# Kernel tuning notes

Hardware: AMD Instinct MI355X
Metric: run time of the kernel (lower is better)

Reference implementation:

```python
import jax, jax.numpy as jnp
import numpy as np

N_NODES = 100000


def gcn_conv(x, edge_index, weight, num_nodes):
    """PyG GCNConv (bias=False): transform -> add self-loops -> sym-normalized scatter-add."""
    h = x @ weight  # [N, out]
    src, dst = edge_index[0], edge_index[1]
    loop = jnp.arange(num_nodes, dtype=src.dtype)
    src = jnp.concatenate([src, loop])
    dst = jnp.concatenate([dst, loop])
    ones = jnp.ones(src.shape[0], dtype=h.dtype)
    deg = jax.ops.segment_sum(ones, dst, num_segments=num_nodes)  # in-degree incl. self-loop
    dis = jnp.where(deg > 0, jax.lax.rsqrt(deg), 0.0)             # deg^-1/2, inf -> 0
    norm = dis[src] * dis[dst]                                    # [E+N]
    msg = norm[:, None] * h[src]                                  # gather + scale
    return jax.ops.segment_sum(msg, dst, num_segments=num_nodes)  # scatter-add


def setup_inputs() -> dict:
    key = jax.random.key(0)
    k1, k2, k3, k4 = jax.random.split(key, 4)
    x = jax.random.normal(k1, (N_NODES, 512), dtype=jnp.float32)
    edge_index = jax.random.randint(k2, (2, 3200000), 0, N_NODES, dtype=jnp.int64)
    weight1 = jax.random.normal(k3, (512, 16), dtype=jnp.float32) * 0.05
    weight2 = jax.random.normal(k4, (16, 16), dtype=jnp.float32) * 0.25
    return {"x": x, "edge_index": edge_index, "weight1": weight1, "weight2": weight2}


def reference(x, edge_index, weight1, weight2):
    n = x.shape[0]
    h = gcn_conv(x, edge_index, weight1, n)
    out = gcn_conv(h, edge_index, weight2, n)
    return out
```

## Files before the change

kernel.cpp:

```cpp
#include <hip/hip_runtime.h>
#include <hip/hip_bf16.h>


#define N_NODES 100000
#define F_IN 512
#define F_OUT 16

__global__ void k_deg_init(float* __restrict__ deg, int n) {
    int i = blockIdx.x * blockDim.x + threadIdx.x;
    if (i < n) deg[i] = 1.0f;
}

__global__ void k_deg_count(const int* __restrict__ dst, float* __restrict__ deg, int E) {
    int e = blockIdx.x * blockDim.x + threadIdx.x;
    if (e < E) unsafeAtomicAdd(&deg[dst[e]], 1.0f);
}

__global__ void k_rsqrt(float* __restrict__ deg, int n) {
    int i = blockIdx.x * blockDim.x + threadIdx.x;
    if (i < n) deg[i] = rsqrtf(deg[i]);
}

__global__ __launch_bounds__(256) void k_gemm1(const float* __restrict__ x,
                                               const float* __restrict__ W,
                                               float* __restrict__ h, int nrows) {
    __shared__ float Ws[F_IN * F_OUT];
    const float4* W4 = (const float4*)W;
    float4* Ws4 = (float4*)Ws;
    for (int i = threadIdx.x; i < (F_IN * F_OUT) / 4; i += 256) Ws4[i] = W4[i];
    __syncthreads();

    int r = blockIdx.x * 16 + (threadIdx.x >> 4);
    int o = threadIdx.x & 15;
    if (r >= nrows) return;

    const float4* xr = (const float4*)(x + (size_t)r * F_IN);
    float acc = 0.0f;
#pragma unroll 8
    for (int k4 = 0; k4 < F_IN / 4; ++k4) {
        float4 xv = xr[k4];
        int k = k4 * 4;
        acc = fmaf(xv.x, Ws[(k + 0) * 16 + o], acc);
        acc = fmaf(xv.y, Ws[(k + 1) * 16 + o], acc);
        acc = fmaf(xv.z, Ws[(k + 2) * 16 + o], acc);
        acc = fmaf(xv.w, Ws[(k + 3) * 16 + o], acc);
    }
    h[(size_t)r * 16 + o] = acc;
}

__global__ void k_selfloop_init(const float* __restrict__ dis,
                                const float* __restrict__ h,
                                float* __restrict__ out, int total) {
    int t = blockIdx.x * blockDim.x + threadIdx.x;
    if (t >= total) return;
    int i = t >> 4;
    float d = dis[i];
    out[t] = d * d * h[t];
}

__global__ __launch_bounds__(256) void k_scatter(const int* __restrict__ src,
                                                 const int* __restrict__ dst,
                                                 const float* __restrict__ dis,
                                                 const float* __restrict__ h,
                                                 float* __restrict__ out, int E) {
    int gid = blockIdx.x * 256 + threadIdx.x;
    int e = gid >> 4;
    if (e >= E) return;
    int c = gid & 15;
    int s = src[e];
    int d = dst[e];
    float norm = dis[s] * dis[d];
    float v = norm * h[(size_t)s * 16 + c];
    unsafeAtomicAdd(&out[(size_t)d * 16 + c], v);
}

__global__ __launch_bounds__(256) void k_gemm2_fused(const float* __restrict__ a,
                                                     const float* __restrict__ W,
                                                     const float* __restrict__ dis,
                                                     float* __restrict__ h2,
                                                     float* __restrict__ out, int nrows) {
    __shared__ float Ws[F_OUT * F_OUT];
    if (threadIdx.x < F_OUT * F_OUT) Ws[threadIdx.x] = W[threadIdx.x];
    __syncthreads();

    int r = blockIdx.x * 16 + (threadIdx.x >> 4);
    int o = threadIdx.x & 15;
    if (r >= nrows) return;

    const float* ar = a + (size_t)r * 16;
    float acc = 0.0f;
#pragma unroll
    for (int k = 0; k < 16; ++k) acc = fmaf(ar[k], Ws[k * 16 + o], acc);

    size_t idx = (size_t)r * 16 + o;
    h2[idx] = acc;
    float d = dis[r];
    out[idx] = d * d * acc;
}

extern "C" void kernel_launch(void* const* d_in, const int* in_sizes, int n_in,
                              void* d_out, int out_size, void* d_ws, size_t ws_size,
                              hipStream_t stream) {
    const float* x  = (const float*)d_in[0];
    const int*   ei = (const int*)d_in[1];
    const float* W1 = (const float*)d_in[2];
    const float* W2 = (const float*)d_in[3];
    float* out = (float*)d_out;

    const int N = N_NODES;
    const int E = in_sizes[1] / 2;
    const int* src = ei;
    const int* dst = ei + E;

    float* ws   = (float*)d_ws;
    float* dis  = ws;
    float* h1   = dis + N;
    float* out1 = h1 + (size_t)N * 16;
    float* h2   = out1 + (size_t)N * 16;

    const int B = 256;
    const int NC = N * F_OUT;

    k_deg_init<<<(N + B - 1) / B, B, 0, stream>>>(dis, N);
    k_deg_count<<<(E + B - 1) / B, B, 0, stream>>>(dst, dis, E);
    k_rsqrt<<<(N + B - 1) / B, B, 0, stream>>>(dis, N);

    k_gemm1<<<(N + 15) / 16, B, 0, stream>>>(x, W1, h1, N);
    k_selfloop_init<<<(NC + B - 1) / B, B, 0, stream>>>(dis, h1, out1, NC);
    {
        long long threads = (long long)E * 16;
        k_scatter<<<(unsigned)((threads + B - 1) / B), B, 0, stream>>>(src, dst, dis, h1, out1, E);
    }

    k_gemm2_fused<<<(N + 15) / 16, B, 0, stream>>>(out1, W2, dis, h2, out, N);
    {
        long long threads = (long long)E * 16;
        k_scatter<<<(unsigned)((threads + B - 1) / B), B, 0, stream>>>(src, dst, dis, h2, out, E);
    }
}
```

Before: 891.2 us.

## Build CSR by destination and replace atomic scatter with pull-based aggregation

Counts integer in-degrees, prefix-scans them into row pointers and fills a destination-sorted source-index array. Each layer then gathers neighbours per node without float atomics, and the self-loop term is folded into the aggregation. GEMM1 is also restructured: each thread loads x coalesced and broadcasts values via shuffles, with W stored transposed and padded in shared memory. Building the CSR costs an extra pass with atomics and workspace, falls back to the old path if the workspace is too small, and per-node loops over roughly 32 neighbours can be imbalanced.

```diff
diff --git a/kernel.cpp b/kernel.cpp
--- a/kernel.cpp
+++ b/kernel.cpp
@@ -5,51 +5,177 @@
 #define N_NODES 100000
 #define F_IN 512
 #define F_OUT 16
+#define WS_PAD 516
+
+__global__ __launch_bounds__(256) void k_gemm1(const float* __restrict__ x,
+                                               const float* __restrict__ W,
+                                               float* __restrict__ h, int nrows) {
+    __shared__ __align__(16) float Ws[F_OUT * WS_PAD];
+    for (int i = threadIdx.x; i < F_IN * F_OUT; i += 256) {
+        int k = i >> 4, o = i & 15;
+        Ws[o * WS_PAD + k] = W[i];
+    }
+    __syncthreads();
+
+    int l = threadIdx.x & 15;
+    int r = blockIdx.x * 16 + (threadIdx.x >> 4);
+    if (r >= nrows) return;
+
+    const float4* xr = (const float4*)(x + (size_t)r * F_IN);
+    float4 v[8];
+#pragma unroll
+    for (int c = 0; c < 8; ++c) v[c] = xr[c * 16 + l];
+
+    const float* wrow = Ws + l * WS_PAD;
+    float acc = 0.0f;
+#pragma unroll
+    for (int c = 0; c < 8; ++c) {
+#pragma unroll
+        for (int t = 0; t < 16; ++t) {
+            float4 wv = *(const float4*)(wrow + c * 64 + t * 4);
+            float ax = __shfl(v[c].x, t, 16);
+            float ay = __shfl(v[c].y, t, 16);
+            float az = __shfl(v[c].z, t, 16);
+            float aw = __shfl(v[c].w, t, 16);
+            acc = fmaf(ax, wv.x, acc);
+            acc = fmaf(ay, wv.y, acc);
+            acc = fmaf(az, wv.z, acc);
+            acc = fmaf(aw, wv.w, acc);
+        }
+    }
+    h[(size_t)r * 16 + l] = acc;
+}
+
+__global__ __launch_bounds__(256) void k_gemm2(const float* __restrict__ a,
+                                               const float* __restrict__ W,
+                                               float* __restrict__ h2, int nrows) {
+    __shared__ float Ws[F_OUT * 17];
+    if (threadIdx.x < 256) {
+        int i = threadIdx.x;
+        int k = i >> 4, o = i & 15;
+        Ws[o * 17 + k] = W[i];
+    }
+    __syncthreads();
+    int l = threadIdx.x & 15;
+    int r = blockIdx.x * 16 + (threadIdx.x >> 4);
+    if (r >= nrows) return;
+    float av = a[(size_t)r * 16 + l];
+    const float* wrow = Ws + l * 17;
+    float acc = 0.0f;
+#pragma unroll
+    for (int t = 0; t < 16; ++t) {
+        float xv = __shfl(av, t, 16);
+        acc = fmaf(xv, wrow[t], acc);
+    }
+    h2[(size_t)r * 16 + l] = acc;
+}
+
+__global__ void k_zero_i32(int* __restrict__ p, int n) {
+    int i = blockIdx.x * blockDim.x + threadIdx.x;
+    if (i < n) p[i] = 0;
+}
+
+__global__ void k_hist(const int* __restrict__ dst, int* __restrict__ deg, int E) {
+    int e = blockIdx.x * blockDim.x + threadIdx.x;
+    if (e < E) atomicAdd(&deg[dst[e]], 1);
+}
+
+__global__ void k_dis(const int* __restrict__ deg, float* __restrict__ dis, int n) {
+    int i = blockIdx.x * blockDim.x + threadIdx.x;
+    if (i < n) dis[i] = rsqrtf(1.0f + (float)deg[i]);
+}
+
+__global__ __launch_bounds__(256) void k_scan1(const int* __restrict__ deg,
+                                               int* __restrict__ rowp,
+                                               int* __restrict__ bsum, int n) {
+    __shared__ int s[256];
+    int i = threadIdx.x;
+    int gi = blockIdx.x * 256 + i;
+    int v = (gi < n) ? deg[gi] : 0;
+    s[i] = v;
+    __syncthreads();
+#pragma unroll
+    for (int off = 1; off < 256; off <<= 1) {
+        int t = (i >= off) ? s[i - off] : 0;
+        __syncthreads();
+        s[i] += t;
+        __syncthreads();
+    }
+    if (gi < n) rowp[gi] = s[i] - v;
+    if (i == 255) bsum[blockIdx.x] = s[255];
+}
+
+__global__ __launch_bounds__(512) void k_scan2(int* __restrict__ bsum, int nb) {
+    __shared__ int s[512];
+    int i = threadIdx.x;
+    int v = (i < nb) ? bsum[i] : 0;
+    s[i] = v;
+    __syncthreads();
+#pragma unroll
+    for (int off = 1; off < 512; off <<= 1) {
+        int t = (i >= off) ? s[i - off] : 0;
+        __syncthreads();
+        s[i] += t;
+        __syncthreads();
+    }
+    if (i < nb) bsum[i] = s[i] - v;
+}
+
+__global__ void k_scan3(int* __restrict__ rowp, int* __restrict__ pos,
+                        const int* __restrict__ bsum, int n, int E) {
+    int gi = blockIdx.x * blockDim.x + threadIdx.x;
+    if (gi < n) {
+        int r = rowp[gi] + bsum[blockIdx.x * blockDim.x / 256 + (threadIdx.x >= 0 ? 0 : 0)];
+        r = rowp[gi] + bsum[gi >> 8];
+        rowp[gi] = r;
+        pos[gi] = r;
+    }
+    if (gi == 0) rowp[n] = E;
+}
+
+__global__ void k_fill(const int* __restrict__ src, const int* __restrict__ dst,
+                       int* __restrict__ pos, int* __restrict__ esrc, int E) {
+    int e = blockIdx.x * blockDim.x + threadIdx.x;
+    if (e < E) {
+        int d = dst[e];
+        int slot = atomicAdd(&pos[d], 1);
+        esrc[slot] = src[e];
+    }
+}
+
+__global__ __launch_bounds__(256) void k_agg(const int* __restrict__ rowp,
+                                             const int* __restrict__ esrc,
+                                             const float* __restrict__ dis,
+                                             const float* __restrict__ h,
+                                             float* __restrict__ out, int n) {
+    int tid = blockIdx.x * 256 + threadIdx.x;
+    int node = tid >> 4;
+    int c = tid & 15;
+    if (node >= n) return;
+    float dd = dis[node];
+    float acc = dd * dd * h[(size_t)node * 16 + c];
+    int b = rowp[node], e = rowp[node + 1];
+    for (int j = b; j < e; ++j) {
+        int s = esrc[j];
+        float w = dd * dis[s];
+        acc = fmaf(w, h[(size_t)s * 16 + c], acc);
+    }
+    out[(size_t)node * 16 + c] = acc;
+}
 
 __global__ void k_deg_init(float* __restrict__ deg, int n) {
     int i = blockIdx.x * blockDim.x + threadIdx.x;
     if (i < n) deg[i] = 1.0f;
 }
-
 __global__ void k_deg_count(const int* __restrict__ dst, float* __restrict__ deg, int E) {
     int e = blockIdx.x * blockDim.x + threadIdx.x;
     if (e < E) unsafeAtomicAdd(&deg[dst[e]], 1.0f);
 }
-
 __global__ void k_rsqrt(float* __restrict__ deg, int n) {
     int i = blockIdx.x * blockDim.x + threadIdx.x;
     if (i < n) deg[i] = rsqrtf(deg[i]);
 }
-
-__global__ __launch_bounds__(256) void k_gemm1(const float* __restrict__ x,
-                                               const float* __restrict__ W,
-                                               float* __restrict__ h, int nrows) {
-    __shared__ float Ws[F_IN * F_OUT];
-    const float4* W4 = (const float4*)W;
-    float4* Ws4 = (float4*)Ws;
-    for (int i = threadIdx.x; i < (F_IN * F_OUT) / 4; i += 256) Ws4[i] = W4[i];
-    __syncthreads();
-
-    int r = blockIdx.x * 16 + (threadIdx.x >> 4);
-    int o = threadIdx.x & 15;
-    if (r >= nrows) return;
-
-    const float4* xr = (const float4*)(x + (size_t)r * F_IN);
-    float acc = 0.0f;
-#pragma unroll 8
-    for (int k4 = 0; k4 < F_IN / 4; ++k4) {
-        float4 xv = xr[k4];
-        int k = k4 * 4;
-        acc = fmaf(xv.x, Ws[(k + 0) * 16 + o], acc);
-        acc = fmaf(xv.y, Ws[(k + 1) * 16 + o], acc);
-        acc = fmaf(xv.z, Ws[(k + 2) * 16 + o], acc);
-        acc = fmaf(xv.w, Ws[(k + 3) * 16 + o], acc);
-    }
-    h[(size_t)r * 16 + o] = acc;
-}
-
-__global__ void k_selfloop_init(const float* __restrict__ dis,
-                                const float* __restrict__ h,
+__global__ void k_selfloop_init(const float* __restrict__ dis, const float* __restrict__ h,
                                 float* __restrict__ out, int total) {
     int t = blockIdx.x * blockDim.x + threadIdx.x;
     if (t >= total) return;
@@ -57,7 +183,6 @@
     float d = dis[i];
     out[t] = d * d * h[t];
 }
-
 __global__ __launch_bounds__(256) void k_scatter(const int* __restrict__ src,
                                                  const int* __restrict__ dst,
                                                  const float* __restrict__ dis,
@@ -69,33 +194,8 @@
     int c = gid & 15;
     int s = src[e];
     int d = dst[e];
-    float norm = dis[s] * dis[d];
-    float v = norm * h[(size_t)s * 16 + c];
+    float v = dis[s] * dis[d] * h[(size_t)s * 16 + c];
     unsafeAtomicAdd(&out[(size_t)d * 16 + c], v);
-}
-
-__global__ __launch_bounds__(256) void k_gemm2_fused(const float* __restrict__ a,
-                                                     const float* __restrict__ W,
-                                                     const float* __restrict__ dis,
-                                                     float* __restrict__ h2,
-                                                     float* __restrict__ out, int nrows) {
-    __shared__ float Ws[F_OUT * F_OUT];
-    if (threadIdx.x < F_OUT * F_OUT) Ws[threadIdx.x] = W[threadIdx.x];
-    __syncthreads();
-
-    int r = blockIdx.x * 16 + (threadIdx.x >> 4);
-    int o = threadIdx.x & 15;
-    if (r >= nrows) return;
-
-    const float* ar = a + (size_t)r * 16;
-    float acc = 0.0f;
-#pragma unroll
-    for (int k = 0; k < 16; ++k) acc = fmaf(ar[k], Ws[k * 16 + o], acc);
-
-    size_t idx = (size_t)r * 16 + o;
-    h2[idx] = acc;
-    float d = dis[r];
-    out[idx] = d * d * acc;
 }
 
 extern "C" void kernel_launch(void* const* d_in, const int* in_sizes, int n_in,
@@ -111,30 +211,54 @@
     const int E = in_sizes[1] / 2;
     const int* src = ei;
     const int* dst = ei + E;
-
-    float* ws   = (float*)d_ws;
-    float* dis  = ws;
-    float* h1   = dis + N;
-    float* out1 = h1 + (size_t)N * 16;
-    float* h2   = out1 + (size_t)N * 16;
-
     const int B = 256;
-    const int NC = N * F_OUT;
-
-    k_deg_init<<<(N + B - 1) / B, B, 0, stream>>>(dis, N);
-    k_deg_count<<<(E + B - 1) / B, B, 0, stream>>>(dst, dis, E);
-    k_rsqrt<<<(N + B - 1) / B, B, 0, stream>>>(dis, N);
-
-    k_gemm1<<<(N + 15) / 16, B, 0, stream>>>(x, W1, h1, N);
-    k_selfloop_init<<<(NC + B - 1) / B, B, 0, stream>>>(dis, h1, out1, NC);
-    {
-        long long threads = (long long)E * 16;
-        k_scatter<<<(unsigned)((threads + B - 1) / B), B, 0, stream>>>(src, dst, dis, h1, out1, E);
-    }
-
-    k_gemm2_fused<<<(N + 15) / 16, B, 0, stream>>>(out1, W2, dis, h2, out, N);
-    {
-        long long threads = (long long)E * 16;
-        k_scatter<<<(unsigned)((threads + B - 1) / B), B, 0, stream>>>(src, dst, dis, h2, out, E);
-    }
-}
+    const int nb = (N + 255) / 256;
+
+    float* dis  = (float*)d_ws;
+    float* bufA = dis + N;
+    float* bufB = bufA + (size_t)N * 16;
+    int* deg  = (int*)(bufB + (size_t)N * 16);
+    int* rowp = deg + N;
+    int* pos  = rowp + (N + 1);
+    int* bsum = pos + N;
+    int* esrc = bsum + 512;
+    size_t needed = (size_t)((char*)(esrc + E) - (char*)d_ws);
+
+    if (ws_size >= needed) {
+        k_zero_i32<<<(N + B - 1) / B, B, 0, stream>>>(deg, N);
+        k_hist<<<(E + B - 1) / B, B, 0, stream>>>(dst, deg, E);
+        k_dis<<<(N + B - 1) / B, B, 0, stream>>>(deg, dis, N);
+        k_scan1<<<nb, 256, 0, stream>>>(deg, rowp, bsum, N);
+        k_scan2<<<1, 512, 0, stream>>>(bsum, nb);
+        k_scan3<<<nb, 256, 0, stream>>>(rowp, pos, bsum, N, E);
+        k_fill<<<(E + B - 1) / B, B, 0, stream>>>(src, dst, pos, esrc, E);
+
+        k_gemm1<<<(N + 15) / 16, B, 0, stream>>>(x, W1, bufA, N);
+        k_agg<<<(N * 16 + B - 1) / B, B, 0, stream>>>(rowp, esrc, dis, bufA, bufB, N);
+        k_gemm2<<<(N + 15) / 16, B, 0, stream>>>(bufB, W2, bufA, N);
+        k_agg<<<(N * 16 + B - 1) / B, B, 0, stream>>>(rowp, esrc, dis, bufA, out, N);
+    } else {
+        float* fdis = (float*)d_ws;
+        float* h1   = fdis + N;
+        float* out1 = h1 + (size_t)N * 16;
+        float* h2   = out1 + (size_t)N * 16;
+        const int NC = N * F_OUT;
+
+        k_deg_init<<<(N + B - 1) / B, B, 0, stream>>>(fdis, N);
+        k_deg_count<<<(E + B - 1) / B, B, 0, stream>>>(dst, fdis, E);
+        k_rsqrt<<<(N + B - 1) / B, B, 0, stream>>>(fdis, N);
+
+        k_gemm1<<<(N + 15) / 16, B, 0, stream>>>(x, W1, h1, N);
+        k_selfloop_init<<<(NC + B - 1) / B, B, 0, stream>>>(fdis, h1, out1, NC);
+        {
+            long long threads = (long long)E * 16;
+            k_scatter<<<(unsigned)((threads + B - 1) / B), B, 0, stream>>>(src, dst, fdis, h1, out1, E);
+        }
+        k_gemm2<<<(N + 15) / 16, B, 0, stream>>>(out1, W2, h2, N);
+        k_selfloop_init<<<(NC + B - 1) / B, B, 0, stream>>>(fdis, h2, out, NC);
+        {
+            long long threads = (long long)E * 16;
+            k_scatter<<<(unsigned)((threads + B - 1) / B), B, 0, stream>>>(src, dst, fdis, h2, out, E);
+        }
+    }
+}
```

New measurement: 980.4 us. +10.0%, slower.

## Fold symmetric normalization into node features and restructure GEMM1 with coalesced loads

Applied to the files above, without the earlier changes.

Factors the edge norm dis[s]*dis[d] so that source-side scaling is applied once per node in the GEMMs and destination-side scaling once per node afterwards. The scatter kernels then no longer gather dis per edge. Degree counting switches to integer atomics with the self-loop added analytically, and the self-loop init kernel is fused into the GEMM epilogue. GEMM1 is rewritten to load x rows coalesced across 16 lanes and broadcast values via shuffles against a transposed, padded weight tile, at the cost of many cross-lane shuffles.

```diff
diff --git a/kernel.cpp b/kernel.cpp
--- a/kernel.cpp
+++ b/kernel.cpp
@@ -5,97 +5,133 @@
 #define N_NODES 100000
 #define F_IN 512
 #define F_OUT 16
+#define WS_PAD 516
 
-__global__ void k_deg_init(float* __restrict__ deg, int n) {
+__global__ void k_zero_i32(int* __restrict__ p, int n) {
     int i = blockIdx.x * blockDim.x + threadIdx.x;
-    if (i < n) deg[i] = 1.0f;
+    if (i < n) p[i] = 0;
 }
 
-__global__ void k_deg_count(const int* __restrict__ dst, float* __restrict__ deg, int E) {
+__global__ void k_hist(const int* __restrict__ dst, int* __restrict__ deg, int E) {
     int e = blockIdx.x * blockDim.x + threadIdx.x;
-    if (e < E) unsafeAtomicAdd(&deg[dst[e]], 1.0f);
+    if (e < E) atomicAdd(&deg[dst[e]], 1);
 }
 
-__global__ void k_rsqrt(float* __restrict__ deg, int n) {
+__global__ void k_dis(const int* __restrict__ deg, float* __restrict__ dis, int n) {
     int i = blockIdx.x * blockDim.x + threadIdx.x;
-    if (i < n) deg[i] = rsqrtf(deg[i]);
+    if (i < n) dis[i] = rsqrtf(1.0f + (float)deg[i]);
 }
 
-__global__ __launch_bounds__(256) void k_gemm1(const float* __restrict__ x,
-                                               const float* __restrict__ W,
-                                               float* __restrict__ h, int nrows) {
-    __shared__ float Ws[F_IN * F_OUT];
-    const float4* W4 = (const float4*)W;
-    float4* Ws4 = (float4*)Ws;
-    for (int i = threadIdx.x; i < (F_IN * F_OUT) / 4; i += 256) Ws4[i] = W4[i];
+__global__ __launch_bounds__(512, 8) void k_gemm1(const float* __restrict__ x,
+                                                  const float* __restrict__ W,
+                                                  const float* __restrict__ dis,
+                                                  float* __restrict__ hw,
+                                                  float* __restrict__ accum,
+                                                  int nrows) {
+    __shared__ __align__(16) float Ws[F_OUT * WS_PAD];
+    for (int i = threadIdx.x; i < F_IN * F_OUT; i += 512) {
+        int k = i >> 4, o = i & 15;
+        Ws[o * WS_PAD + k] = W[i];
+    }
     __syncthreads();
 
-    int r = blockIdx.x * 16 + (threadIdx.x >> 4);
-    int o = threadIdx.x & 15;
+    int l = threadIdx.x & 15;
+    int r = blockIdx.x * 32 + (threadIdx.x >> 4);
     if (r >= nrows) return;
 
     const float4* xr = (const float4*)(x + (size_t)r * F_IN);
-    float acc = 0.0f;
-#pragma unroll 8
-    for (int k4 = 0; k4 < F_IN / 4; ++k4) {
-        float4 xv = xr[k4];
-        int k = k4 * 4;
-        acc = fmaf(xv.x, Ws[(k + 0) * 16 + o], acc);
-        acc = fmaf(xv.y, Ws[(k + 1) * 16 + o], acc);
-        acc = fmaf(xv.z, Ws[(k + 2) * 16 + o], acc);
-        acc = fmaf(xv.w, Ws[(k + 3) * 16 + o], acc);
+    const float* wrow = Ws + l * WS_PAD;
+    float acc0 = 0.0f, acc1 = 0.0f;
+
+#pragma unroll
+    for (int half = 0; half < 2; ++half) {
+        float4 v0 = xr[half * 64 + 0 * 16 + l];
+        float4 v1 = xr[half * 64 + 1 * 16 + l];
+        float4 v2 = xr[half * 64 + 2 * 16 + l];
+        float4 v3 = xr[half * 64 + 3 * 16 + l];
+        const float* wb = wrow + half * 256;
+#pragma unroll
+        for (int t = 0; t < 16; ++t) {
+            float4 wa = *(const float4*)(wb + t * 4);
+            float4 wc = *(const float4*)(wb + 64 + t * 4);
+            acc0 = fmaf(__shfl(v0.x, t, 16), wa.x, acc0);
+            acc0 = fmaf(__shfl(v0.y, t, 16), wa.y, acc0);
+            acc0 = fmaf(__shfl(v0.z, t, 16), wa.z, acc0);
+            acc0 = fmaf(__shfl(v0.w, t, 16), wa.w, acc0);
+            acc1 = fmaf(__shfl(v1.x, t, 16), wc.x, acc1);
+            acc1 = fmaf(__shfl(v1.y, t, 16), wc.y, acc1);
+            acc1 = fmaf(__shfl(v1.z, t, 16), wc.z, acc1);
+            acc1 = fmaf(__shfl(v1.w, t, 16), wc.w, acc1);
+        }
+#pragma unroll
+        for (int t = 0; t < 16; ++t) {
+            float4 wa = *(const float4*)(wb + 128 + t * 4);
+            float4 wc = *(const float4*)(wb + 192 + t * 4);
+            acc0 = fmaf(__shfl(v2.x, t, 16), wa.x, acc0);
+            acc0 = fmaf(__shfl(v2.y, t, 16), wa.y, acc0);
+            acc0 = fmaf(__shfl(v2.z, t, 16), wa.z, acc0);
+            acc0 = fmaf(__shfl(v2.w, t, 16), wa.w, acc0);
+            acc1 = fmaf(__shfl(v3.x, t, 16), wc.x, acc1);
+            acc1 = fmaf(__shfl(v3.y, t, 16), wc.y, acc1);
+            acc1 = fmaf(__shfl(v3.z, t, 16), wc.z, acc1);
+            acc1 = fmaf(__shfl(v3.w, t, 16), wc.w, acc1);
+        }
     }
-    h[(size_t)r * 16 + o] = acc;
+    float hv = dis[r] * (acc0 + acc1);
+    size_t o = (size_t)r * 16 + l;
+    hw[o] = hv;
+    accum[o] = hv;
 }
 
-__global__ void k_selfloop_init(const float* __restrict__ dis,
-                                const float* __restrict__ h,
-                                float* __restrict__ out, int total) {
-    int t = blockIdx.x * blockDim.x + threadIdx.x;
-    if (t >= total) return;
-    int i = t >> 4;
-    float d = dis[i];
-    out[t] = d * d * h[t];
+__global__ __launch_bounds__(256) void k_gemm2(const float* __restrict__ S1,
+                                               const float* __restrict__ W,
+                                               const float* __restrict__ dis,
+                                               float* __restrict__ hw2,
+                                               float* __restrict__ accum,
+                                               int nrows) {
+    __shared__ float Ws[F_OUT * 17];
+    if (threadIdx.x < 256) {
+        int i = threadIdx.x;
+        int k = i >> 4, o = i & 15;
+        Ws[o * 17 + k] = W[i];
+    }
+    __syncthreads();
+    int l = threadIdx.x & 15;
+    int r = blockIdx.x * 16 + (threadIdx.x >> 4);
+    if (r >= nrows) return;
+    float dr = dis[r];
+    float av = dr * S1[(size_t)r * 16 + l];
+    const float* wrow = Ws + l * 17;
+    float acc = 0.0f;
+#pragma unroll
+    for (int t = 0; t < 16; ++t) {
+        float xv = __shfl(av, t, 16);
+        acc = fmaf(xv, wrow[t], acc);
+    }
+    float hv = dr * acc;
+    size_t o = (size_t)r * 16 + l;
+    hw2[o] = hv;
+    accum[o] = hv;
 }
 
 __global__ __launch_bounds__(256) void k_scatter(const int* __restrict__ src,
                                                  const int* __restrict__ dst,
-                                                 const float* __restrict__ dis,
-                                                 const float* __restrict__ h,
-                                                 float* __restrict__ out, int E) {
+                                                 const float* __restrict__ hw,
+                                                 float* __restrict__ accum, int E) {
     int gid = blockIdx.x * 256 + threadIdx.x;
     int e = gid >> 4;
     if (e >= E) return;
     int c = gid & 15;
     int s = src[e];
     int d = dst[e];
-    float norm = dis[s] * dis[d];
-    float v = norm * h[(size_t)s * 16 + c];
-    unsafeAtomicAdd(&out[(size_t)d * 16 + c], v);
+    float v = hw[(size_t)s * 16 + c];
+    unsafeAtomicAdd(&accum[(size_t)d * 16 + c], v);
 }
 
-__global__ __launch_bounds__(256) void k_gemm2_fused(const float* __restrict__ a,
-                                                     const float* __restrict__ W,
-                                                     const float* __restrict__ dis,
-                                                     float* __restrict__ h2,
-                                                     float* __restrict__ out, int nrows) {
-    __shared__ float Ws[F_OUT * F_OUT];
-    if (threadIdx.x < F_OUT * F_OUT) Ws[threadIdx.x] = W[threadIdx.x];
-    __syncthreads();
-
-    int r = blockIdx.x * 16 + (threadIdx.x >> 4);
-    int o = threadIdx.x & 15;
-    if (r >= nrows) return;
-
-    const float* ar = a + (size_t)r * 16;
-    float acc = 0.0f;
-#pragma unroll
-    for (int k = 0; k < 16; ++k) acc = fmaf(ar[k], Ws[k * 16 + o], acc);
-
-    size_t idx = (size_t)r * 16 + o;
-    h2[idx] = acc;
-    float d = dis[r];
-    out[idx] = d * d * acc;
+__global__ void k_scale(float* __restrict__ out, const float* __restrict__ dis, int total) {
+    int t = blockIdx.x * blockDim.x + threadIdx.x;
+    if (t >= total) return;
+    out[t] *= dis[t >> 4];
 }
 
 extern "C" void kernel_launch(void* const* d_in, const int* in_sizes, int n_in,
@@ -111,30 +147,28 @@
     const int E = in_sizes[1] / 2;
     const int* src = ei;
     const int* dst = ei + E;
-
-    float* ws   = (float*)d_ws;
-    float* dis  = ws;
-    float* h1   = dis + N;
-    float* out1 = h1 + (size_t)N * 16;
-    float* h2   = out1 + (size_t)N * 16;
-
     const int B = 256;
     const int NC = N * F_OUT;
 
-    k_deg_init<<<(N + B - 1) / B, B, 0, stream>>>(dis, N);
-    k_deg_count<<<(E + B - 1) / B, B, 0, stream>>>(dst, dis, E);
-    k_rsqrt<<<(N + B - 1) / B, B, 0, stream>>>(dis, N);
+    float* dis  = (float*)d_ws;
+    float* bufA = dis + N;
+    float* bufB = bufA + (size_t)N * 16;
+    int*   deg  = (int*)(bufB + (size_t)N * 16);
 
-    k_gemm1<<<(N + 15) / 16, B, 0, stream>>>(x, W1, h1, N);
-    k_selfloop_init<<<(NC + B - 1) / B, B, 0, stream>>>(dis, h1, out1, NC);
+    k_zero_i32<<<(N + B - 1) / B, B, 0, stream>>>(deg, N);
+    k_hist<<<(E + B - 1) / B, B, 0, stream>>>(dst, deg, E);
+    k_dis<<<(N + B - 1) / B, B, 0, stream>>>(deg, dis, N);
+
+    k_gemm1<<<(N + 31) / 32, 512, 0, stream>>>(x, W1, dis, bufA, bufB, N);
     {
         long long threads = (long long)E * 16;
-        k_scatter<<<(unsigned)((threads + B - 1) / B), B, 0, stream>>>(src, dst, dis, h1, out1, E);
+        k_scatter<<<(unsigned)((threads + B - 1) / B), B, 0, stream>>>(src, dst, bufA, bufB, E);
     }
 
-    k_gemm2_fused<<<(N + 15) / 16, B, 0, stream>>>(out1, W2, dis, h2, out, N);
+    k_gemm2<<<(N + 15) / 16, B, 0, stream>>>(bufB, W2, dis, bufA, out, N);
     {
         long long threads = (long long)E * 16;
-        k_scatter<<<(unsigned)((threads + B - 1) / B), B, 0, stream>>>(src, dst, dis, h2, out, E);
+        k_scatter<<<(unsigned)((threads + B - 1) / B), B, 0, stream>>>(src, dst, bufA, out, E);
     }
+    k_scale<<<(NC + B - 1) / B, B, 0, stream>>>(out, dis, NC);
 }
```

New measurement: 861.3 us. 1.03x faster.
